# Kernel optimization log

Hardware: AMD Instinct MI355X
Metric: run time of the kernel (lower is better)

Reference implementation:

```python
import jax, jax.numpy as jnp
import numpy as np

NG, ND, NC, H = 100000, 50000, 50000, 128

def _sage(x_src, x_dst, src, dst, n_dst, W_l, b_l, W_r):
    # PyG SAGEConv: lin_l(mean over incoming neighbors of x_src) + lin_r(x_dst)
    msg = x_src[src]                                             # [E, H] gather
    s = jax.ops.segment_sum(msg, dst, num_segments=n_dst)        # [n_dst, H]
    cnt = jax.ops.segment_sum(jnp.ones(src.shape, x_src.dtype), dst, num_segments=n_dst)
    mean = s / jnp.maximum(cnt, 1.0)[:, None]
    return mean @ W_l + b_l + x_dst @ W_r


def setup_inputs() -> dict:
    key = jax.random.key(0)
    ks = jax.random.split(key, 12)
    sc = 1.0 / np.sqrt(H)
    return {
        'emb_gene': jax.random.normal(ks[0], (NG, H), jnp.float32) * 0.02,
        'emb_disease': jax.random.normal(ks[1], (ND, H), jnp.float32) * 0.02,
        'emb_compound': jax.random.normal(ks[2], (NC, H), jnp.float32) * 0.02,
        'Wl': jax.random.normal(ks[3], (2, 4, H, H), jnp.float32) * sc,
        'bl': jnp.zeros((2, 4, H), jnp.float32),
        'Wr': jax.random.normal(ks[4], (2, 4, H, H), jnp.float32) * sc,
        'eg_src': jax.random.randint(ks[5], (600000,), 0, NG),
        'eg_dst': jax.random.randint(ks[6], (600000,), 0, NG),
        'ecd_src': jax.random.randint(ks[7], (300000,), 0, NC),
        'ecd_dst': jax.random.randint(ks[8], (300000,), 0, ND),
        'ecg_src': jax.random.randint(ks[9], (600000,), 0, NC),
        'ecg_dst': jax.random.randint(ks[10], (600000,), 0, NG),
        'egc_src': jax.random.randint(ks[11], (600000,), 0, NG),
        'egc_dst': jax.random.randint(jax.random.fold_in(key, 99), (600000,), 0, NC),
    }


def reference(emb_gene, emb_disease, emb_compound, Wl, bl, Wr,
              eg_src, eg_dst, ecd_src, ecd_dst, ecg_src, ecg_dst, egc_src, egc_dst):
    xg, xd, xc = emb_gene, emb_disease, emb_compound
    for L in range(2):
        # to_hetero with aggr='sum': sum per-relation SAGEConv outputs per dst type
        og = (_sage(xg, xg, eg_src, eg_dst, NG, Wl[L, 0], bl[L, 0], Wr[L, 0]) +
              _sage(xc, xg, ecg_src, ecg_dst, NG, Wl[L, 2], bl[L, 2], Wr[L, 2]))
        od = _sage(xc, xd, ecd_src, ecd_dst, ND, Wl[L, 1], bl[L, 1], Wr[L, 1])
        oc = _sage(xg, xc, egc_src, egc_dst, NC, Wl[L, 3], bl[L, 3], Wr[L, 3])
        if L < 1:  # relu between layers (dropout inactive in eval)
            og, od, oc = jax.nn.relu(og), jax.nn.relu(od), jax.nn.relu(oc)
        xg, xd, xc = og, od, oc
    # concatenate node-type outputs [NG+ND+NC, H] for a single output array
    return jnp.concatenate([xg, xd, xc], axis=0)
```

## Files before the change

kernel.cpp:

```cpp
#include <hip/hip_runtime.h>


constexpr int HD = 128;
constexpr int NBMAX = 512;
constexpr int BSTRIDE = 32768;

typedef __attribute__((ext_vector_type(8))) short bf16x8;
typedef __attribute__((ext_vector_type(16))) float f32x16;
typedef __attribute__((ext_vector_type(2))) float f32x2;

__device__ __forceinline__ unsigned short f2bf(float x) {
  unsigned u = __builtin_bit_cast(unsigned, x);
  u += 0x7FFF + ((u >> 16) & 1);
  return (unsigned short)(u >> 16);
}
__device__ __forceinline__ float bf2f(unsigned short h) {
  return __builtin_bit_cast(float, (unsigned)h << 16);
}

__device__ __forceinline__ uint2 pack_fp8x8(const float* v) {
  uint2 o;
  unsigned t;
  t = (unsigned)__builtin_amdgcn_cvt_pk_fp8_f32(v[0] * 16.f, v[1] * 16.f, 0, false);
  t = (unsigned)__builtin_amdgcn_cvt_pk_fp8_f32(v[2] * 16.f, v[3] * 16.f, (int)t, true);
  o.x = t;
  t = (unsigned)__builtin_amdgcn_cvt_pk_fp8_f32(v[4] * 16.f, v[5] * 16.f, 0, false);
  t = (unsigned)__builtin_amdgcn_cvt_pk_fp8_f32(v[6] * 16.f, v[7] * 16.f, (int)t, true);
  o.y = t;
  return o;
}

__global__ __launch_bounds__(256) void k_convert(const float* __restrict__ s0,
                                                 const float* __restrict__ s1,
                                                 const float* __restrict__ s2,
                                                 unsigned short* __restrict__ d0,
                                                 unsigned short* __restrict__ d1,
                                                 unsigned short* __restrict__ d2,
                                                 unsigned char* __restrict__ e0,
                                                 unsigned char* __restrict__ e2,
                                                 long long n0, long long n1, long long n2) {
  long long i = ((long long)blockIdx.x * 256 + threadIdx.x) * 8;
  const float* s;
  unsigned short* d;
  unsigned char* e;
  if (i < n0) { s = s0 + i; d = d0 + i; e = e0 + i; }
  else if (i < n0 + n1) { s = s1 + (i - n0); d = d1 + (i - n0); e = nullptr; }
  else if (i < n0 + n1 + n2) { s = s2 + (i - n0 - n1); d = d2 + (i - n0 - n1); e = e2 + (i - n0 - n1); }
  else return;
  float4 a = *(const float4*)s;
  float4 b = *(const float4*)(s + 4);
  float v[8] = {a.x, a.y, a.z, a.w, b.x, b.y, b.z, b.w};
  uint4 o;
  o.x = (unsigned)f2bf(v[0]) | ((unsigned)f2bf(v[1]) << 16);
  o.y = (unsigned)f2bf(v[2]) | ((unsigned)f2bf(v[3]) << 16);
  o.z = (unsigned)f2bf(v[4]) | ((unsigned)f2bf(v[5]) << 16);
  o.w = (unsigned)f2bf(v[6]) | ((unsigned)f2bf(v[7]) << 16);
  *(uint4*)d = o;
  if (e) *(uint2*)e = pack_fp8x8(v);
}

struct GArgs {
  const int* esrc[4];
  const int* edst[4];
  int ebase[5];
  int nbase[4];
};

__global__ __launch_bounds__(256) void k_binA(GArgs ga, int Etot, int NB,
                                              int* __restrict__ bucketCur,
                                              unsigned* __restrict__ binned) {
  __shared__ int hist[NBMAX];
  __shared__ int base[NBMAX];
  const int tid = threadIdx.x;
  for (int b = tid; b < NB; b += 256) hist[b] = 0;
  __syncthreads();
  const int e0 = blockIdx.x * 4096;
  for (int i = tid; i < 4096; i += 256) {
    int e = e0 + i;
    if (e < Etot) {
      int r = (e >= ga.ebase[1]) + (e >= ga.ebase[2]) + (e >= ga.ebase[3]);
      int g = ga.nbase[r] + ga.edst[r][e - ga.ebase[r]];
      atomicAdd(&hist[g >> 10], 1);
    }
  }
  __syncthreads();
  for (int b = tid; b < NB; b += 256) {
    int h = hist[b];
    base[b] = h ? atomicAdd(&bucketCur[b], h) : 0;
    hist[b] = 0;
  }
  __syncthreads();
  for (int i = tid; i < 4096; i += 256) {
    int e = e0 + i;
    if (e < Etot) {
      int r = (e >= ga.ebase[1]) + (e >= ga.ebase[2]) + (e >= ga.ebase[3]);
      int el = e - ga.ebase[r];
      int g = ga.nbase[r] + ga.edst[r][el];
      int b = g >> 10;
      int pos = base[b] + atomicAdd(&hist[b], 1);
      binned[(size_t)b * BSTRIDE + pos] =
          ((unsigned)(g & 1023) << 20) | (unsigned)ga.esrc[r][el];
    }
  }
}

__global__ __launch_bounds__(256) void k_binB(const int* __restrict__ bucketCur,
                                              const unsigned* __restrict__ binned,
                                              int* __restrict__ ptr, int* __restrict__ cnt,
                                              int* __restrict__ ss, int Ntot) {
  const int b = blockIdx.x;
  const int tid = threadIdx.x;
  __shared__ int ncnt[1024];
  __shared__ int noff[1024];
  __shared__ int red[256];
  __shared__ int sbase_s;
  __shared__ int wsum[4], wbase[4];

  int part = 0;
  for (int i = tid; i < b; i += 256) part += bucketCur[i];
  red[tid] = part;
  __syncthreads();
  for (int s = 128; s > 0; s >>= 1) {
    if (tid < s) red[tid] += red[tid + s];
    __syncthreads();
  }
  if (tid == 0) sbase_s = red[0];

  for (int j = tid; j < 1024; j += 256) ncnt[j] = 0;
  __syncthreads();

  const int ecount = bucketCur[b];
  const unsigned* bp = binned + (size_t)b * BSTRIDE;
  for (int i = tid; i < ecount; i += 256) atomicAdd(&ncnt[bp[i] >> 20], 1);
  __syncthreads();

  const int j0 = tid * 4;
  int c0 = ncnt[j0], c1 = ncnt[j0 + 1], c2 = ncnt[j0 + 2], c3 = ncnt[j0 + 3];
  int s4 = c0 + c1 + c2 + c3;
  int lane = tid & 63, wid = tid >> 6;
  int incl = s4;
#pragma unroll
  for (int off = 1; off < 64; off <<= 1) {
    int t = __shfl_up(incl, off);
    if (lane >= off) incl += t;
  }
  if (lane == 63) wsum[wid] = incl;
  __syncthreads();
  if (tid == 0) {
    int acc = 0;
#pragma unroll
    for (int w2 = 0; w2 < 4; ++w2) { wbase[w2] = acc; acc += wsum[w2]; }
  }
  __syncthreads();
  int excl = wbase[wid] + incl - s4;
  const int sbase = sbase_s;
  int o0 = excl, o1 = excl + c0, o2 = o1 + c1, o3 = o2 + c2;
  noff[j0] = o0; noff[j0 + 1] = o1; noff[j0 + 2] = o2; noff[j0 + 3] = o3;
  int g0 = b * 1024 + j0;
  if (g0 + 0 < Ntot) { ptr[g0 + 0] = sbase + o0; cnt[g0 + 0] = c0; }
  if (g0 + 1 < Ntot) { ptr[g0 + 1] = sbase + o1; cnt[g0 + 1] = c1; }
  if (g0 + 2 < Ntot) { ptr[g0 + 2] = sbase + o2; cnt[g0 + 2] = c2; }
  if (g0 + 3 < Ntot) { ptr[g0 + 3] = sbase + o3; cnt[g0 + 3] = c3; }
  __syncthreads();

  for (int i = tid; i < ecount; i += 256) {
    unsigned rec = bp[i];
    int j = rec >> 20;
    int p = sbase + atomicAdd(&noff[j], 1);
    ss[p] = (int)(rec & 0xFFFFF);
  }
}

struct AArgs {
  const unsigned char* xs[4];
  unsigned short* mean[4];
  int nbase[4];
  int bbase[5];
  int n[4];
};

__global__ __launch_bounds__(256) void k_aggregate_all(AArgs A, const int* __restrict__ ptr,
                                                       const int* __restrict__ cnt,
                                                       const int* __restrict__ ss) {
  int b = blockIdx.x;
  int r = (b >= A.bbase[1]) + (b >= A.bbase[2]) + (b >= A.bbase[3]);
  int d = (b - A.bbase[r]) * 32 + (threadIdx.x >> 3);
  if (d >= A.n[r]) return;
  const unsigned char* xs = A.xs[r];
  int l = threadIdx.x & 7;
  int g = A.nbase[r] + d;
  int p = ptr[g];
  int deg = cnt[g];
  f32x2 b0 = {0.f, 0.f}, b1 = {0.f, 0.f}, b2 = {0.f, 0.f}, b3 = {0.f, 0.f};
  f32x2 b4 = {0.f, 0.f}, b5 = {0.f, 0.f}, b6 = {0.f, 0.f}, b7 = {0.f, 0.f};
  for (int j0 = 0; j0 < deg; j0 += 8) {
    int m = deg - j0;
    if (m > 8) m = 8;
    int idx = ss[p + j0 + (l < m ? l : m - 1)];
    uint4 uu[8];
#pragma unroll
    for (int k = 0; k < 8; ++k) {
      if (k < m) {
        int s = __shfl(idx, k, 8);
        uu[k] = *(const uint4*)(xs + (size_t)s * HD + l * 16);
      }
    }
#pragma unroll
    for (int k = 0; k < 8; ++k) {
      if (k < m) {
        b0 += __builtin_amdgcn_cvt_pk_f32_fp8(uu[k].x, false);
        b1 += __builtin_amdgcn_cvt_pk_f32_fp8(uu[k].x, true);
        b2 += __builtin_amdgcn_cvt_pk_f32_fp8(uu[k].y, false);
        b3 += __builtin_amdgcn_cvt_pk_f32_fp8(uu[k].y, true);
        b4 += __builtin_amdgcn_cvt_pk_f32_fp8(uu[k].z, false);
        b5 += __builtin_amdgcn_cvt_pk_f32_fp8(uu[k].z, true);
        b6 += __builtin_amdgcn_cvt_pk_f32_fp8(uu[k].w, false);
        b7 += __builtin_amdgcn_cvt_pk_f32_fp8(uu[k].w, true);
      }
    }
  }
  float inv = 1.0f / (16.0f * (float)(deg > 0 ? deg : 1));
  uint4 o;
  unsigned short* mp = A.mean[r] + (size_t)d * HD + l * 16;
  o.x = (unsigned)f2bf(b0.x * inv) | ((unsigned)f2bf(b0.y * inv) << 16);
  o.y = (unsigned)f2bf(b1.x * inv) | ((unsigned)f2bf(b1.y * inv) << 16);
  o.z = (unsigned)f2bf(b2.x * inv) | ((unsigned)f2bf(b2.y * inv) << 16);
  o.w = (unsigned)f2bf(b3.x * inv) | ((unsigned)f2bf(b3.y * inv) << 16);
  *(uint4*)mp = o;
  o.x = (unsigned)f2bf(b4.x * inv) | ((unsigned)f2bf(b4.y * inv) << 16);
  o.y = (unsigned)f2bf(b5.x * inv) | ((unsigned)f2bf(b5.y * inv) << 16);
  o.z = (unsigned)f2bf(b6.x * inv) | ((unsigned)f2bf(b6.y * inv) << 16);
  o.w = (unsigned)f2bf(b7.x * inv) | ((unsigned)f2bf(b7.y * inv) << 16);
  *(uint4*)(mp + 8) = o;
}

struct PrepArgs {
  const float* a[14];
  const float* b[14];
};

__global__ __launch_bounds__(256) void k_prepw(PrepArgs pa, unsigned short* __restrict__ out) {
  int s = blockIdx.x;
  const float* A = pa.a[s];
  const float* B = pa.b[s];
  unsigned short* oh = out + (size_t)s * 16384;
  int e0 = blockIdx.y * 1024 + threadIdx.x * 4;
#pragma unroll
  for (int j = 0; j < 4; ++j) {
    int e = e0 + j;
    int k = e >> 7, n = e & 127;
    float v = A[e] + (B ? B[e] : 0.f);
    oh[n * 128 + (k ^ ((n & 15) << 3))] = f2bf(v);
  }
}

struct GemmArgs {
  const unsigned short* x[3][3];
  const unsigned short* wp[3][3];
  const float* b0[3];
  const float* b1[3];
  float* outf[3];
  unsigned short* outb[3];
  unsigned char* out8[3];
  int M[3];
  int nslab[3];
  int gbase[4];
  int relu;
};

__global__ __launch_bounds__(256, 4) void k_gemm_all(GemmArgs ga) {
  __shared__ unsigned short ldsb[16384];
  const int t = (blockIdx.x >= ga.gbase[1]) + (blockIdx.x >= ga.gbase[2]);
  const int blk = blockIdx.x - ga.gbase[t];
  const int M = ga.M[t];
  const int nslab = ga.nslab[t];
  const int tid = threadIdx.x;
  const int wave = tid >> 6;
  const int lane = tid & 63;
  const int l31 = lane & 31;
  const int lhalf = lane >> 5;

  const int mbase = blk * 128 + wave * 32;
  int r0 = mbase + l31;
  if (r0 > M - 1) r0 = M - 1;

  f32x16 acc[4];
#pragma unroll
  for (int n = 0; n < 4; ++n)
#pragma unroll
    for (int q = 0; q < 16; ++q) acc[n][q] = 0.f;

#pragma unroll
  for (int s = 0; s < 3; ++s) {
    if (s < nslab) {
      const unsigned short* xp = ga.x[t][s] + (size_t)r0 * HD + lhalf * 8;
      bf16x8 areg[8];
#pragma unroll
      for (int ks = 0; ks < 8; ++ks) areg[ks] = *(const bf16x8*)(xp + ks * 16);

      __syncthreads();
      {
        const float4* src = (const float4*)ga.wp[t][s];
        float4* dst = (float4*)ldsb;
#pragma unroll
        for (int j = 0; j < 8; ++j) dst[tid + j * 256] = src[tid + j * 256];
      }
      __syncthreads();

#pragma unroll
      for (int ks = 0; ks < 8; ++ks) {
        const int k0 = ks * 16 + lhalf * 8;
#pragma unroll
        for (int nt = 0; nt < 4; ++nt) {
          const int rown = nt * 32 + l31;
          const int kidx = k0 ^ ((rown & 15) << 3);
          const bf16x8 bb = *(const bf16x8*)&ldsb[rown * HD + kidx];
          acc[nt] = __builtin_amdgcn_mfma_f32_32x32x16_bf16(areg[ks], bb, acc[nt], 0, 0, 0);
        }
      }
    }
  }

  const float* b0 = ga.b0[t];
  const float* b1 = ga.b1[t];
  float* outf = ga.outf[t];
  unsigned short* outb = ga.outb[t];
  unsigned char* out8 = ga.out8[t];
#pragma unroll
  for (int nt = 0; nt < 4; ++nt) {
    const int col = nt * 32 + l31;
    float bias = b0[col] + (b1 ? b1[col] : 0.f);
#pragma unroll
    for (int rg = 0; rg < 16; ++rg) {
      int row = mbase + (rg & 3) + 8 * (rg >> 2) + 4 * lhalf;
      float v = acc[nt][rg] + bias;
      if (ga.relu) v = fmaxf(v, 0.f);
      if (row < M) {
        if (outf) {
          outf[(size_t)row * HD + col] = v;
        } else {
          unsigned short h = f2bf(v);
          outb[(size_t)row * HD + col] = h;
          if (out8) {
            float vb = bf2f(h);
            unsigned pk = (unsigned)__builtin_amdgcn_cvt_pk_fp8_f32(vb * 16.f, vb * 16.f, 0, false);
            out8[(size_t)row * HD + col] = (unsigned char)(pk & 0xFF);
          }
        }
      }
    }
  }
}

extern "C" void kernel_launch(void* const* d_in, const int* in_sizes, int n_in,
                              void* d_out, int out_size, void* d_ws, size_t ws_size,
                              hipStream_t stream) {
  const float* emb_g = (const float*)d_in[0];
  const float* emb_d = (const float*)d_in[1];
  const float* emb_c = (const float*)d_in[2];
  const float* Wl = (const float*)d_in[3];
  const float* bl = (const float*)d_in[4];
  const float* Wr = (const float*)d_in[5];

  const int NG = in_sizes[0] / HD;
  const int ND = in_sizes[1] / HD;
  const int NC = in_sizes[2] / HD;
  const int E0 = in_sizes[6];
  const int E1 = in_sizes[8];
  const int E2 = in_sizes[10];
  const int E3 = in_sizes[12];
  const int HH = HD * HD;
  const int Etot = E0 + E1 + E2 + E3;
  const int Ntot = NG + ND + NG + NC;
  const int NB = (Ntot + 1023) >> 10;

  char* w = (char*)d_ws;
  unsigned short* wprep = (unsigned short*)w; w += (size_t)14 * 32768;
  unsigned short* xbf_g0 = (unsigned short*)w; w += (size_t)NG * HD * 2;
  unsigned short* xbf_d0 = (unsigned short*)w; w += (size_t)ND * HD * 2;
  unsigned short* xbf_c0 = (unsigned short*)w; w += (size_t)NC * HD * 2;
  unsigned short* xbf_g1 = (unsigned short*)w; w += (size_t)NG * HD * 2;
  unsigned short* xbf_d1 = (unsigned short*)w; w += (size_t)ND * HD * 2;
  unsigned short* xbf_c1 = (unsigned short*)w; w += (size_t)NC * HD * 2;
  unsigned short* mean_gg = (unsigned short*)w; w += (size_t)NG * HD * 2;
  unsigned short* mean_cd = (unsigned short*)w; w += (size_t)ND * HD * 2;
  unsigned short* mean_cg = (unsigned short*)w; w += (size_t)NG * HD * 2;
  unsigned short* mean_gc = (unsigned short*)w; w += (size_t)NC * HD * 2;
  unsigned char* x8_g0 = (unsigned char*)w; w += (size_t)NG * HD;
  unsigned char* x8_c0 = (unsigned char*)w; w += (size_t)NC * HD;
  unsigned char* x8_g1 = (unsigned char*)w; w += (size_t)NG * HD;
  unsigned char* x8_c1 = (unsigned char*)w; w += (size_t)NC * HD;
  int* ss = (int*)w;        w += (size_t)Etot * 4;
  int* ptr = (int*)w;       w += (size_t)Ntot * 4;
  int* cnt = (int*)w;       w += (size_t)Ntot * 4;
  unsigned* binned = (unsigned*)w; w += (size_t)NB * BSTRIDE * 4;
  int* bucketCur = (int*)w; w += (size_t)NBMAX * 4;

  hipMemsetAsync(bucketCur, 0, (size_t)NBMAX * 4, stream);

  {
    long long n0 = (long long)NG * HD, n1 = (long long)ND * HD, n2 = (long long)NC * HD;
    long long tot8 = (n0 + n1 + n2) / 8;
    k_convert<<<(int)((tot8 + 255) / 256), 256, 0, stream>>>(
        emb_g, emb_d, emb_c, xbf_g0, xbf_d0, xbf_c0, x8_g0, x8_c0, n0, n1, n2);
  }

  GArgs ga;
  ga.esrc[0] = (const int*)d_in[6];  ga.edst[0] = (const int*)d_in[7];
  ga.esrc[1] = (const int*)d_in[8];  ga.edst[1] = (const int*)d_in[9];
  ga.esrc[2] = (const int*)d_in[10]; ga.edst[2] = (const int*)d_in[11];
  ga.esrc[3] = (const int*)d_in[12]; ga.edst[3] = (const int*)d_in[13];
  ga.ebase[0] = 0; ga.ebase[1] = E0; ga.ebase[2] = E0 + E1;
  ga.ebase[3] = E0 + E1 + E2; ga.ebase[4] = Etot;
  ga.nbase[0] = 0; ga.nbase[1] = NG; ga.nbase[2] = NG + ND; ga.nbase[3] = NG + ND + NG;

  k_binA<<<(Etot + 4095) / 4096, 256, 0, stream>>>(ga, Etot, NB, bucketCur, binned);
  k_binB<<<NB, 256, 0, stream>>>(bucketCur, binned, ptr, cnt, ss, Ntot);

  PrepArgs pa;
  for (int L = 0; L < 2; ++L) {
    int b = L * 7;
    pa.a[b + 0] = Wl + (size_t)(L * 4 + 0) * HH; pa.b[b + 0] = nullptr;
    pa.a[b + 1] = Wl + (size_t)(L * 4 + 2) * HH; pa.b[b + 1] = nullptr;
    pa.a[b + 2] = Wr + (size_t)(L * 4 + 0) * HH; pa.b[b + 2] = Wr + (size_t)(L * 4 + 2) * HH;
    pa.a[b + 3] = Wl + (size_t)(L * 4 + 1) * HH; pa.b[b + 3] = nullptr;
    pa.a[b + 4] = Wr + (size_t)(L * 4 + 1) * HH; pa.b[b + 4] = nullptr;
    pa.a[b + 5] = Wl + (size_t)(L * 4 + 3) * HH; pa.b[b + 5] = nullptr;
    pa.a[b + 6] = Wr + (size_t)(L * 4 + 3) * HH; pa.b[b + 6] = nullptr;
  }
  k_prepw<<<dim3(14, 16), 256, 0, stream>>>(pa, wprep);

  float* out = (float*)d_out;
  float* xg_out = out;
  float* xd_out = out + (size_t)NG * HD;
  float* xc_out = out + (size_t)(NG + ND) * HD;

  for (int L = 0; L < 2; ++L) {
    const unsigned short* xg = L ? xbf_g1 : xbf_g0;
    const unsigned short* xd = L ? xbf_d1 : xbf_d0;
    const unsigned short* xc = L ? xbf_c1 : xbf_c0;
    const unsigned char* x8g = L ? x8_g1 : x8_g0;
    const unsigned char* x8c = L ? x8_c1 : x8_c0;

    AArgs aa;
    aa.xs[0] = x8g; aa.xs[1] = x8c; aa.xs[2] = x8c; aa.xs[3] = x8g;
    aa.mean[0] = mean_gg; aa.mean[1] = mean_cd; aa.mean[2] = mean_cg; aa.mean[3] = mean_gc;
    aa.nbase[0] = 0; aa.nbase[1] = NG; aa.nbase[2] = NG + ND; aa.nbase[3] = NG + ND + NG;
    aa.n[0] = NG; aa.n[1] = ND; aa.n[2] = NG; aa.n[3] = NC;
    int bb = 0;
    for (int r = 0; r < 4; ++r) { aa.bbase[r] = bb; bb += (aa.n[r] + 31) / 32; }
    aa.bbase[4] = bb;
    k_aggregate_all<<<bb, 256, 0, stream>>>(aa, ptr, cnt, ss);

    const float* bl_L = bl + (size_t)L * 4 * HD;
    const unsigned short* wp = wprep + (size_t)L * 7 * 16384;

    GemmArgs gm;
    gm.x[0][0] = mean_gg; gm.x[0][1] = mean_cg; gm.x[0][2] = xg;
    gm.wp[0][0] = wp + 0 * 16384; gm.wp[0][1] = wp + 1 * 16384; gm.wp[0][2] = wp + 2 * 16384;
    gm.b0[0] = bl_L + 0 * HD; gm.b1[0] = bl_L + 2 * HD;
    gm.M[0] = NG; gm.nslab[0] = 3;
    gm.x[1][0] = mean_cd; gm.x[1][1] = xd; gm.x[1][2] = nullptr;
    gm.wp[1][0] = wp + 3 * 16384; gm.wp[1][1] = wp + 4 * 16384; gm.wp[1][2] = nullptr;
    gm.b0[1] = bl_L + 1 * HD; gm.b1[1] = nullptr;
    gm.M[1] = ND; gm.nslab[1] = 2;
    gm.x[2][0] = mean_gc; gm.x[2][1] = xc; gm.x[2][2] = nullptr;
    gm.wp[2][0] = wp + 5 * 16384; gm.wp[2][1] = wp + 6 * 16384; gm.wp[2][2] = nullptr;
    gm.b0[2] = bl_L + 3 * HD; gm.b1[2] = nullptr;
    gm.M[2] = NC; gm.nslab[2] = 2;
    if (L) {
      gm.outf[0] = xg_out; gm.outf[1] = xd_out; gm.outf[2] = xc_out;
      gm.outb[0] = gm.outb[1] = gm.outb[2] = nullptr;
      gm.out8[0] = gm.out8[1] = gm.out8[2] = nullptr;
    } else {
      gm.outf[0] = gm.outf[1] = gm.outf[2] = nullptr;
      gm.outb[0] = xbf_g1; gm.outb[1] = xbf_d1; gm.outb[2] = xbf_c1;
      gm.out8[0] = x8_g1; gm.out8[1] = nullptr; gm.out8[2] = x8_c1;
    }
    gm.relu = (L == 0) ? 1 : 0;
    int gb = 0;
    for (int t = 0; t < 3; ++t) { gm.gbase[t] = gb; gb += (gm.M[t] + 127) / 128; }
    gm.gbase[3] = gb;
    k_gemm_all<<<gb, 256, 0, stream>>>(gm);
  }
}
```

Measured before the change: 334.1 us.

## Fuse front-end kernels, pad CSR segments for vectorized index loads

Merges the embedding conversion, edge binning pass A, and weight prep into a single k_front launch distinguished by block ranges, removing two launches and letting them overlap. The CSR built in k_binB now pads each node's neighbor segment to a multiple of 8 and aligns each bucket base, so the aggregation kernel can read 8 source indices with two uint4 loads instead of a strided load plus shuffles. Aggregated mean rows are written with nontemporal stores. The padding enlarges the index buffer and reads slightly past valid entries for partial groups, which are masked by m.

After: 331.8 us. No clear change (-0.7%).

```diff
diff --git a/kernel.cpp b/kernel.cpp
--- a/kernel.cpp
+++ b/kernel.cpp
@@ -4,10 +4,12 @@
 constexpr int HD = 128;
 constexpr int NBMAX = 512;
 constexpr int BSTRIDE = 32768;
+constexpr int PADRES = 7176;
 
 typedef __attribute__((ext_vector_type(8))) short bf16x8;
 typedef __attribute__((ext_vector_type(16))) float f32x16;
 typedef __attribute__((ext_vector_type(2))) float f32x2;
+typedef __attribute__((ext_vector_type(4))) unsigned int u32x4;
 
 __device__ __forceinline__ unsigned short f2bf(float x) {
   unsigned u = __builtin_bit_cast(unsigned, x);
@@ -30,35 +32,6 @@
   return o;
 }
 
-__global__ __launch_bounds__(256) void k_convert(const float* __restrict__ s0,
-                                                 const float* __restrict__ s1,
-                                                 const float* __restrict__ s2,
-                                                 unsigned short* __restrict__ d0,
-                                                 unsigned short* __restrict__ d1,
-                                                 unsigned short* __restrict__ d2,
-                                                 unsigned char* __restrict__ e0,
-                                                 unsigned char* __restrict__ e2,
-                                                 long long n0, long long n1, long long n2) {
-  long long i = ((long long)blockIdx.x * 256 + threadIdx.x) * 8;
-  const float* s;
-  unsigned short* d;
-  unsigned char* e;
-  if (i < n0) { s = s0 + i; d = d0 + i; e = e0 + i; }
-  else if (i < n0 + n1) { s = s1 + (i - n0); d = d1 + (i - n0); e = nullptr; }
-  else if (i < n0 + n1 + n2) { s = s2 + (i - n0 - n1); d = d2 + (i - n0 - n1); e = e2 + (i - n0 - n1); }
-  else return;
-  float4 a = *(const float4*)s;
-  float4 b = *(const float4*)(s + 4);
-  float v[8] = {a.x, a.y, a.z, a.w, b.x, b.y, b.z, b.w};
-  uint4 o;
-  o.x = (unsigned)f2bf(v[0]) | ((unsigned)f2bf(v[1]) << 16);
-  o.y = (unsigned)f2bf(v[2]) | ((unsigned)f2bf(v[3]) << 16);
-  o.z = (unsigned)f2bf(v[4]) | ((unsigned)f2bf(v[5]) << 16);
-  o.w = (unsigned)f2bf(v[6]) | ((unsigned)f2bf(v[7]) << 16);
-  *(uint4*)d = o;
-  if (e) *(uint2*)e = pack_fp8x8(v);
-}
-
 struct GArgs {
   const int* esrc[4];
   const int* edst[4];
@@ -66,41 +39,102 @@
   int nbase[4];
 };
 
-__global__ __launch_bounds__(256) void k_binA(GArgs ga, int Etot, int NB,
-                                              int* __restrict__ bucketCur,
-                                              unsigned* __restrict__ binned) {
+struct PrepArgs {
+  const float* a[14];
+  const float* b[14];
+};
+
+struct FrontArgs {
+  const float *cs0, *cs1, *cs2;
+  unsigned short *cd0, *cd1, *cd2;
+  unsigned char *ce0, *ce2;
+  long long n0, n1, n2;
+  GArgs ga;
+  int Etot, NB;
+  int* bucketCur;
+  unsigned* binned;
+  PrepArgs pa;
+  unsigned short* wprep;
+  int cb, ab;
+};
+
+__global__ __launch_bounds__(256) void k_front(FrontArgs f) {
   __shared__ int hist[NBMAX];
   __shared__ int base[NBMAX];
   const int tid = threadIdx.x;
-  for (int b = tid; b < NB; b += 256) hist[b] = 0;
-  __syncthreads();
-  const int e0 = blockIdx.x * 4096;
-  for (int i = tid; i < 4096; i += 256) {
-    int e = e0 + i;
-    if (e < Etot) {
-      int r = (e >= ga.ebase[1]) + (e >= ga.ebase[2]) + (e >= ga.ebase[3]);
-      int g = ga.nbase[r] + ga.edst[r][e - ga.ebase[r]];
-      atomicAdd(&hist[g >> 10], 1);
-    }
-  }
-  __syncthreads();
-  for (int b = tid; b < NB; b += 256) {
-    int h = hist[b];
-    base[b] = h ? atomicAdd(&bucketCur[b], h) : 0;
-    hist[b] = 0;
-  }
-  __syncthreads();
-  for (int i = tid; i < 4096; i += 256) {
-    int e = e0 + i;
-    if (e < Etot) {
-      int r = (e >= ga.ebase[1]) + (e >= ga.ebase[2]) + (e >= ga.ebase[3]);
-      int el = e - ga.ebase[r];
-      int g = ga.nbase[r] + ga.edst[r][el];
-      int b = g >> 10;
-      int pos = base[b] + atomicAdd(&hist[b], 1);
-      binned[(size_t)b * BSTRIDE + pos] =
-          ((unsigned)(g & 1023) << 20) | (unsigned)ga.esrc[r][el];
-    }
+  int b = blockIdx.x;
+
+  if (b < f.cb) {
+    long long i = ((long long)b * 256 + tid) * 8;
+    const float* s;
+    unsigned short* d;
+    unsigned char* e;
+    if (i < f.n0) { s = f.cs0 + i; d = f.cd0 + i; e = f.ce0 + i; }
+    else if (i < f.n0 + f.n1) { s = f.cs1 + (i - f.n0); d = f.cd1 + (i - f.n0); e = nullptr; }
+    else if (i < f.n0 + f.n1 + f.n2) {
+      long long o2 = i - f.n0 - f.n1;
+      s = f.cs2 + o2; d = f.cd2 + o2; e = f.ce2 + o2;
+    } else return;
+    float4 a = *(const float4*)s;
+    float4 bb = *(const float4*)(s + 4);
+    float v[8] = {a.x, a.y, a.z, a.w, bb.x, bb.y, bb.z, bb.w};
+    uint4 o;
+    o.x = (unsigned)f2bf(v[0]) | ((unsigned)f2bf(v[1]) << 16);
+    o.y = (unsigned)f2bf(v[2]) | ((unsigned)f2bf(v[3]) << 16);
+    o.z = (unsigned)f2bf(v[4]) | ((unsigned)f2bf(v[5]) << 16);
+    o.w = (unsigned)f2bf(v[6]) | ((unsigned)f2bf(v[7]) << 16);
+    *(uint4*)d = o;
+    if (e) *(uint2*)e = pack_fp8x8(v);
+    return;
+  }
+  b -= f.cb;
+
+  if (b < f.ab) {
+    for (int j = tid; j < f.NB; j += 256) hist[j] = 0;
+    __syncthreads();
+    const int e0 = b * 4096;
+    for (int i = tid; i < 4096; i += 256) {
+      int e = e0 + i;
+      if (e < f.Etot) {
+        int r = (e >= f.ga.ebase[1]) + (e >= f.ga.ebase[2]) + (e >= f.ga.ebase[3]);
+        int g = f.ga.nbase[r] + f.ga.edst[r][e - f.ga.ebase[r]];
+        atomicAdd(&hist[g >> 10], 1);
+      }
+    }
+    __syncthreads();
+    for (int j = tid; j < f.NB; j += 256) {
+      int h = hist[j];
+      base[j] = h ? atomicAdd(&f.bucketCur[j], h) : 0;
+      hist[j] = 0;
+    }
+    __syncthreads();
+    for (int i = tid; i < 4096; i += 256) {
+      int e = e0 + i;
+      if (e < f.Etot) {
+        int r = (e >= f.ga.ebase[1]) + (e >= f.ga.ebase[2]) + (e >= f.ga.ebase[3]);
+        int el = e - f.ga.ebase[r];
+        int g = f.ga.nbase[r] + f.ga.edst[r][el];
+        int bk = g >> 10;
+        int pos = base[bk] + atomicAdd(&hist[bk], 1);
+        f.binned[(size_t)bk * BSTRIDE + pos] =
+            ((unsigned)(g & 1023) << 20) | (unsigned)f.ga.esrc[r][el];
+      }
+    }
+    return;
+  }
+  b -= f.ab;
+
+  int s = b >> 4, y = b & 15;
+  const float* A = f.pa.a[s];
+  const float* B = f.pa.b[s];
+  unsigned short* oh = f.wprep + (size_t)s * 16384;
+  int e0 = y * 1024 + tid * 4;
+#pragma unroll
+  for (int j = 0; j < 4; ++j) {
+    int e = e0 + j;
+    int k = e >> 7, n = e & 127;
+    float v = A[e] + (B ? B[e] : 0.f);
+    oh[n * 128 + (k ^ ((n & 15) << 3))] = f2bf(v);
   }
 }
 
@@ -124,7 +158,7 @@
     if (tid < s) red[tid] += red[tid + s];
     __syncthreads();
   }
-  if (tid == 0) sbase_s = red[0];
+  if (tid == 0) sbase_s = ((red[0] + 7) & ~7) + b * PADRES;
 
   for (int j = tid; j < 1024; j += 256) ncnt[j] = 0;
   __syncthreads();
@@ -136,7 +170,8 @@
 
   const int j0 = tid * 4;
   int c0 = ncnt[j0], c1 = ncnt[j0 + 1], c2 = ncnt[j0 + 2], c3 = ncnt[j0 + 3];
-  int s4 = c0 + c1 + c2 + c3;
+  int p0 = (c0 + 7) & ~7, p1 = (c1 + 7) & ~7, p2 = (c2 + 7) & ~7, p3 = (c3 + 7) & ~7;
+  int s4 = p0 + p1 + p2 + p3;
   int lane = tid & 63, wid = tid >> 6;
   int incl = s4;
 #pragma unroll
@@ -154,7 +189,7 @@
   __syncthreads();
   int excl = wbase[wid] + incl - s4;
   const int sbase = sbase_s;
-  int o0 = excl, o1 = excl + c0, o2 = o1 + c1, o3 = o2 + c2;
+  int o0 = excl, o1 = o0 + p0, o2 = o1 + p1, o3 = o2 + p2;
   noff[j0] = o0; noff[j0 + 1] = o1; noff[j0 + 2] = o2; noff[j0 + 3] = o3;
   int g0 = b * 1024 + j0;
   if (g0 + 0 < Ntot) { ptr[g0 + 0] = sbase + o0; cnt[g0 + 0] = c0; }
@@ -196,15 +231,18 @@
   for (int j0 = 0; j0 < deg; j0 += 8) {
     int m = deg - j0;
     if (m > 8) m = 8;
-    int idx = ss[p + j0 + (l < m ? l : m - 1)];
+    const uint4* ip = (const uint4*)(ss + p + j0);
+    uint4 ia = ip[0];
+    uint4 ib = ip[1];
     uint4 uu[8];
-#pragma unroll
-    for (int k = 0; k < 8; ++k) {
-      if (k < m) {
-        int s = __shfl(idx, k, 8);
-        uu[k] = *(const uint4*)(xs + (size_t)s * HD + l * 16);
-      }
-    }
+    if (m > 0) uu[0] = *(const uint4*)(xs + (size_t)ia.x * HD + l * 16);
+    if (m > 1) uu[1] = *(const uint4*)(xs + (size_t)ia.y * HD + l * 16);
+    if (m > 2) uu[2] = *(const uint4*)(xs + (size_t)ia.z * HD + l * 16);
+    if (m > 3) uu[3] = *(const uint4*)(xs + (size_t)ia.w * HD + l * 16);
+    if (m > 4) uu[4] = *(const uint4*)(xs + (size_t)ib.x * HD + l * 16);
+    if (m > 5) uu[5] = *(const uint4*)(xs + (size_t)ib.y * HD + l * 16);
+    if (m > 6) uu[6] = *(const uint4*)(xs + (size_t)ib.z * HD + l * 16);
+    if (m > 7) uu[7] = *(const uint4*)(xs + (size_t)ib.w * HD + l * 16);
 #pragma unroll
     for (int k = 0; k < 8; ++k) {
       if (k < m) {
@@ -220,38 +258,18 @@
     }
   }
   float inv = 1.0f / (16.0f * (float)(deg > 0 ? deg : 1));
-  uint4 o;
+  u32x4 o;
   unsigned short* mp = A.mean[r] + (size_t)d * HD + l * 16;
   o.x = (unsigned)f2bf(b0.x * inv) | ((unsigned)f2bf(b0.y * inv) << 16);
   o.y = (unsigned)f2bf(b1.x * inv) | ((unsigned)f2bf(b1.y * inv) << 16);
   o.z = (unsigned)f2bf(b2.x * inv) | ((unsigned)f2bf(b2.y * inv) << 16);
   o.w = (unsigned)f2bf(b3.x * inv) | ((unsigned)f2bf(b3.y * inv) << 16);
-  *(uint4*)mp = o;
+  __builtin_nontemporal_store(o, (u32x4*)mp);
   o.x = (unsigned)f2bf(b4.x * inv) | ((unsigned)f2bf(b4.y * inv) << 16);
   o.y = (unsigned)f2bf(b5.x * inv) | ((unsigned)f2bf(b5.y * inv) << 16);
   o.z = (unsigned)f2bf(b6.x * inv) | ((unsigned)f2bf(b6.y * inv) << 16);
   o.w = (unsigned)f2bf(b7.x * inv) | ((unsigned)f2bf(b7.y * inv) << 16);
-  *(uint4*)(mp + 8) = o;
-}
-
-struct PrepArgs {
-  const float* a[14];
-  const float* b[14];
-};
-
-__global__ __launch_bounds__(256) void k_prepw(PrepArgs pa, unsigned short* __restrict__ out) {
-  int s = blockIdx.x;
-  const float* A = pa.a[s];
-  const float* B = pa.b[s];
-  unsigned short* oh = out + (size_t)s * 16384;
-  int e0 = blockIdx.y * 1024 + threadIdx.x * 4;
-#pragma unroll
-  for (int j = 0; j < 4; ++j) {
-    int e = e0 + j;
-    int k = e >> 7, n = e & 127;
-    float v = A[e] + (B ? B[e] : 0.f);
-    oh[n * 128 + (k ^ ((n & 15) << 3))] = f2bf(v);
-  }
+  __builtin_nontemporal_store(o, (u32x4*)(mp + 8));
 }
 
 struct GemmArgs {
@@ -390,7 +408,7 @@
   unsigned char* x8_c0 = (unsigned char*)w; w += (size_t)NC * HD;
   unsigned char* x8_g1 = (unsigned char*)w; w += (size_t)NG * HD;
   unsigned char* x8_c1 = (unsigned char*)w; w += (size_t)NC * HD;
-  int* ss = (int*)w;        w += (size_t)Etot * 4;
+  int* ss = (int*)w;        w += ((size_t)Etot + (size_t)NB * PADRES + 64) * 4;
   int* ptr = (int*)w;       w += (size_t)Ntot * 4;
   int* cnt = (int*)w;       w += (size_t)Ntot * 4;
   unsigned* binned = (unsigned*)w; w += (size_t)NB * BSTRIDE * 4;
@@ -398,37 +416,37 @@
 
   hipMemsetAsync(bucketCur, 0, (size_t)NBMAX * 4, stream);
 
-  {
-    long long n0 = (long long)NG * HD, n1 = (long long)ND * HD, n2 = (long long)NC * HD;
-    long long tot8 = (n0 + n1 + n2) / 8;
-    k_convert<<<(int)((tot8 + 255) / 256), 256, 0, stream>>>(
-        emb_g, emb_d, emb_c, xbf_g0, xbf_d0, xbf_c0, x8_g0, x8_c0, n0, n1, n2);
-  }
-
-  GArgs ga;
-  ga.esrc[0] = (const int*)d_in[6];  ga.edst[0] = (const int*)d_in[7];
-  ga.esrc[1] = (const int*)d_in[8];  ga.edst[1] = (const int*)d_in[9];
-  ga.esrc[2] = (const int*)d_in[10]; ga.edst[2] = (const int*)d_in[11];
-  ga.esrc[3] = (const int*)d_in[12]; ga.edst[3] = (const int*)d_in[13];
-  ga.ebase[0] = 0; ga.ebase[1] = E0; ga.ebase[2] = E0 + E1;
-  ga.ebase[3] = E0 + E1 + E2; ga.ebase[4] = Etot;
-  ga.nbase[0] = 0; ga.nbase[1] = NG; ga.nbase[2] = NG + ND; ga.nbase[3] = NG + ND + NG;
-
-  k_binA<<<(Etot + 4095) / 4096, 256, 0, stream>>>(ga, Etot, NB, bucketCur, binned);
-  k_binB<<<NB, 256, 0, stream>>>(bucketCur, binned, ptr, cnt, ss, Ntot);
-
-  PrepArgs pa;
+  FrontArgs fa;
+  fa.cs0 = emb_g; fa.cs1 = emb_d; fa.cs2 = emb_c;
+  fa.cd0 = xbf_g0; fa.cd1 = xbf_d0; fa.cd2 = xbf_c0;
+  fa.ce0 = x8_g0; fa.ce2 = x8_c0;
+  fa.n0 = (long long)NG * HD; fa.n1 = (long long)ND * HD; fa.n2 = (long long)NC * HD;
+  fa.ga.esrc[0] = (const int*)d_in[6];  fa.ga.edst[0] = (const int*)d_in[7];
+  fa.ga.esrc[1] = (const int*)d_in[8];  fa.ga.edst[1] = (const int*)d_in[9];
+  fa.ga.esrc[2] = (const int*)d_in[10]; fa.ga.edst[2] = (const int*)d_in[11];
+  fa.ga.esrc[3] = (const int*)d_in[12]; fa.ga.edst[3] = (const int*)d_in[13];
+  fa.ga.ebase[0] = 0; fa.ga.ebase[1] = E0; fa.ga.ebase[2] = E0 + E1;
+  fa.ga.ebase[3] = E0 + E1 + E2; fa.ga.ebase[4] = Etot;
+  fa.ga.nbase[0] = 0; fa.ga.nbase[1] = NG; fa.ga.nbase[2] = NG + ND; fa.ga.nbase[3] = NG + ND + NG;
+  fa.Etot = Etot; fa.NB = NB;
+  fa.bucketCur = bucketCur; fa.binned = binned;
   for (int L = 0; L < 2; ++L) {
     int b = L * 7;
-    pa.a[b + 0] = Wl + (size_t)(L * 4 + 0) * HH; pa.b[b + 0] = nullptr;
-    pa.a[b + 1] = Wl + (size_t)(L * 4 + 2) * HH; pa.b[b + 1] = nullptr;
-    pa.a[b + 2] = Wr + (size_t)(L * 4 + 0) * HH; pa.b[b + 2] = Wr + (size_t)(L * 4 + 2) * HH;
-    pa.a[b + 3] = Wl + (size_t)(L * 4 + 1) * HH; pa.b[b + 3] = nullptr;
-    pa.a[b + 4] = Wr + (size_t)(L * 4 + 1) * HH; pa.b[b + 4] = nullptr;
-    pa.a[b + 5] = Wl + (size_t)(L * 4 + 3) * HH; pa.b[b + 5] = nullptr;
-    pa.a[b + 6] = Wr + (size_t)(L * 4 + 3) * HH; pa.b[b + 6] = nullptr;
-  }
-  k_prepw<<<dim3(14, 16), 256, 0, stream>>>(pa, wprep);
+    fa.pa.a[b + 0] = Wl + (size_t)(L * 4 + 0) * HH; fa.pa.b[b + 0] = nullptr;
+    fa.pa.a[b + 1] = Wl + (size_t)(L * 4 + 2) * HH; fa.pa.b[b + 1] = nullptr;
+    fa.pa.a[b + 2] = Wr + (size_t)(L * 4 + 0) * HH; fa.pa.b[b + 2] = Wr + (size_t)(L * 4 + 2) * HH;
+    fa.pa.a[b + 3] = Wl + (size_t)(L * 4 + 1) * HH; fa.pa.b[b + 3] = nullptr;
+    fa.pa.a[b + 4] = Wr + (size_t)(L * 4 + 1) * HH; fa.pa.b[b + 4] = nullptr;
+    fa.pa.a[b + 5] = Wl + (size_t)(L * 4 + 3) * HH; fa.pa.b[b + 5] = nullptr;
+    fa.pa.a[b + 6] = Wr + (size_t)(L * 4 + 3) * HH; fa.pa.b[b + 6] = nullptr;
+  }
+  fa.wprep = wprep;
+  long long tot8 = (fa.n0 + fa.n1 + fa.n2) / 8;
+  fa.cb = (int)((tot8 + 255) / 256);
+  fa.ab = (Etot + 4095) / 4096;
+  k_front<<<fa.cb + fa.ab + 14 * 16, 256, 0, stream>>>(fa);
+
+  k_binB<<<NB, 256, 0, stream>>>(bucketCur, binned, ptr, cnt, ss, Ntot);
 
   float* out = (float*)d_out;
   float* xg_out = out;
```

## Shard bucket counters, pad per-node edge lists, vector-load neighbor indices

Applied to the files above, without the earlier changes.

The binning pass now spreads each bucket's global atomic counter over 8 slots with separate sub-regions, rotates the bucket visiting order per block, and processes 8192 edges per block, all to cut atomic contention on the bucket counters. The CSR layout pads each node's neighbor list to a multiple of 8 and aligns each bucket base, so the aggregate kernel can fetch 8 source indices with two uint4 loads instead of a load plus shuffles. The mean outputs are written with nontemporal stores. In exchange the index array grows with padding, and each sub-slot is capped at 4096 edges per bucket, which could overflow on skewed inputs.

After: 364.6 us. +9.1%, slower.

```diff
diff --git a/kernel.cpp b/kernel.cpp
--- a/kernel.cpp
+++ b/kernel.cpp
@@ -4,10 +4,14 @@
 constexpr int HD = 128;
 constexpr int NBMAX = 512;
 constexpr int BSTRIDE = 32768;
+constexpr int SUBSTRIDE = 4096;
+constexpr int EPB = 8192;
+constexpr int PADRES = 7176;
 
 typedef __attribute__((ext_vector_type(8))) short bf16x8;
 typedef __attribute__((ext_vector_type(16))) float f32x16;
 typedef __attribute__((ext_vector_type(2))) float f32x2;
+typedef __attribute__((ext_vector_type(4))) unsigned int u32x4;
 
 __device__ __forceinline__ unsigned short f2bf(float x) {
   unsigned u = __builtin_bit_cast(unsigned, x);
@@ -72,10 +76,11 @@
   __shared__ int hist[NBMAX];
   __shared__ int base[NBMAX];
   const int tid = threadIdx.x;
-  for (int b = tid; b < NB; b += 256) hist[b] = 0;
-  __syncthreads();
-  const int e0 = blockIdx.x * 4096;
-  for (int i = tid; i < 4096; i += 256) {
+  const int slot = blockIdx.x & 7;
+  for (int j = tid; j < NB; j += 256) hist[j] = 0;
+  __syncthreads();
+  const int e0 = blockIdx.x * EPB;
+  for (int i = tid; i < EPB; i += 256) {
     int e = e0 + i;
     if (e < Etot) {
       int r = (e >= ga.ebase[1]) + (e >= ga.ebase[2]) + (e >= ga.ebase[3]);
@@ -84,21 +89,23 @@
     }
   }
   __syncthreads();
-  for (int b = tid; b < NB; b += 256) {
-    int h = hist[b];
-    base[b] = h ? atomicAdd(&bucketCur[b], h) : 0;
-    hist[b] = 0;
-  }
-  __syncthreads();
-  for (int i = tid; i < 4096; i += 256) {
+  const int roff = (int)((blockIdx.x * 67u) % (unsigned)NB);
+  for (int j = tid; j < NB; j += 256) {
+    int jj = j + roff; if (jj >= NB) jj -= NB;
+    int h = hist[jj];
+    base[jj] = h ? atomicAdd(&bucketCur[slot * NBMAX + jj], h) : 0;
+    hist[jj] = 0;
+  }
+  __syncthreads();
+  for (int i = tid; i < EPB; i += 256) {
     int e = e0 + i;
     if (e < Etot) {
       int r = (e >= ga.ebase[1]) + (e >= ga.ebase[2]) + (e >= ga.ebase[3]);
       int el = e - ga.ebase[r];
       int g = ga.nbase[r] + ga.edst[r][el];
-      int b = g >> 10;
-      int pos = base[b] + atomicAdd(&hist[b], 1);
-      binned[(size_t)b * BSTRIDE + pos] =
+      int bk = g >> 10;
+      int pos = base[bk] + atomicAdd(&hist[bk], 1);
+      binned[(size_t)bk * BSTRIDE + slot * SUBSTRIDE + pos] =
           ((unsigned)(g & 1023) << 20) | (unsigned)ga.esrc[r][el];
     }
   }
@@ -117,26 +124,32 @@
   __shared__ int wsum[4], wbase[4];
 
   int part = 0;
-  for (int i = tid; i < b; i += 256) part += bucketCur[i];
+#pragma unroll
+  for (int s = 0; s < 8; ++s)
+    for (int i = tid; i < b; i += 256) part += bucketCur[s * NBMAX + i];
   red[tid] = part;
   __syncthreads();
   for (int s = 128; s > 0; s >>= 1) {
     if (tid < s) red[tid] += red[tid + s];
     __syncthreads();
   }
-  if (tid == 0) sbase_s = red[0];
+  if (tid == 0) sbase_s = ((red[0] + 7) & ~7) + b * PADRES;
 
   for (int j = tid; j < 1024; j += 256) ncnt[j] = 0;
   __syncthreads();
 
-  const int ecount = bucketCur[b];
-  const unsigned* bp = binned + (size_t)b * BSTRIDE;
-  for (int i = tid; i < ecount; i += 256) atomicAdd(&ncnt[bp[i] >> 20], 1);
+#pragma unroll
+  for (int s = 0; s < 8; ++s) {
+    int c = bucketCur[s * NBMAX + b];
+    const unsigned* bps = binned + (size_t)b * BSTRIDE + s * SUBSTRIDE;
+    for (int i = tid; i < c; i += 256) atomicAdd(&ncnt[bps[i] >> 20], 1);
+  }
   __syncthreads();
 
   const int j0 = tid * 4;
   int c0 = ncnt[j0], c1 = ncnt[j0 + 1], c2 = ncnt[j0 + 2], c3 = ncnt[j0 + 3];
-  int s4 = c0 + c1 + c2 + c3;
+  int p0 = (c0 + 7) & ~7, p1 = (c1 + 7) & ~7, p2 = (c2 + 7) & ~7, p3 = (c3 + 7) & ~7;
+  int s4 = p0 + p1 + p2 + p3;
   int lane = tid & 63, wid = tid >> 6;
   int incl = s4;
 #pragma unroll
@@ -154,7 +167,7 @@
   __syncthreads();
   int excl = wbase[wid] + incl - s4;
   const int sbase = sbase_s;
-  int o0 = excl, o1 = excl + c0, o2 = o1 + c1, o3 = o2 + c2;
+  int o0 = excl, o1 = o0 + p0, o2 = o1 + p1, o3 = o2 + p2;
   noff[j0] = o0; noff[j0 + 1] = o1; noff[j0 + 2] = o2; noff[j0 + 3] = o3;
   int g0 = b * 1024 + j0;
   if (g0 + 0 < Ntot) { ptr[g0 + 0] = sbase + o0; cnt[g0 + 0] = c0; }
@@ -163,11 +176,36 @@
   if (g0 + 3 < Ntot) { ptr[g0 + 3] = sbase + o3; cnt[g0 + 3] = c3; }
   __syncthreads();
 
-  for (int i = tid; i < ecount; i += 256) {
-    unsigned rec = bp[i];
-    int j = rec >> 20;
-    int p = sbase + atomicAdd(&noff[j], 1);
-    ss[p] = (int)(rec & 0xFFFFF);
+#pragma unroll
+  for (int s = 0; s < 8; ++s) {
+    int c = bucketCur[s * NBMAX + b];
+    const unsigned* bps = binned + (size_t)b * BSTRIDE + s * SUBSTRIDE;
+    for (int i = tid; i < c; i += 256) {
+      unsigned rec = bps[i];
+      int j = rec >> 20;
+      int p = sbase + atomicAdd(&noff[j], 1);
+      ss[p] = (int)(rec & 0xFFFFF);
+    }
+  }
+}
+
+struct PrepArgs {
+  const float* a[14];
+  const float* b[14];
+};
+
+__global__ __launch_bounds__(256) void k_prepw(PrepArgs pa, unsigned short* __restrict__ out) {
+  int s = blockIdx.x;
+  const float* A = pa.a[s];
+  const float* B = pa.b[s];
+  unsigned short* oh = out + (size_t)s * 16384;
+  int e0 = blockIdx.y * 1024 + threadIdx.x * 4;
+#pragma unroll
+  for (int j = 0; j < 4; ++j) {
+    int e = e0 + j;
+    int k = e >> 7, n = e & 127;
+    float v = A[e] + (B ? B[e] : 0.f);
+    oh[n * 128 + (k ^ ((n & 15) << 3))] = f2bf(v);
   }
 }
 
@@ -196,15 +234,18 @@
   for (int j0 = 0; j0 < deg; j0 += 8) {
     int m = deg - j0;
     if (m > 8) m = 8;
-    int idx = ss[p + j0 + (l < m ? l : m - 1)];
+    const uint4* ip = (const uint4*)(ss + p + j0);
+    uint4 ia = ip[0];
+    uint4 ib = ip[1];
     uint4 uu[8];
-#pragma unroll
-    for (int k = 0; k < 8; ++k) {
-      if (k < m) {
-        int s = __shfl(idx, k, 8);
-        uu[k] = *(const uint4*)(xs + (size_t)s * HD + l * 16);
-      }
-    }
+    if (m > 0) uu[0] = *(const uint4*)(xs + (size_t)ia.x * HD + l * 16);
+    if (m > 1) uu[1] = *(const uint4*)(xs + (size_t)ia.y * HD + l * 16);
+    if (m > 2) uu[2] = *(const uint4*)(xs + (size_t)ia.z * HD + l * 16);
+    if (m > 3) uu[3] = *(const uint4*)(xs + (size_t)ia.w * HD + l * 16);
+    if (m > 4) uu[4] = *(const uint4*)(xs + (size_t)ib.x * HD + l * 16);
+    if (m > 5) uu[5] = *(const uint4*)(xs + (size_t)ib.y * HD + l * 16);
+    if (m > 6) uu[6] = *(const uint4*)(xs + (size_t)ib.z * HD + l * 16);
+    if (m > 7) uu[7] = *(const uint4*)(xs + (size_t)ib.w * HD + l * 16);
 #pragma unroll
     for (int k = 0; k < 8; ++k) {
       if (k < m) {
@@ -220,38 +261,18 @@
     }
   }
   float inv = 1.0f / (16.0f * (float)(deg > 0 ? deg : 1));
-  uint4 o;
+  u32x4 o;
   unsigned short* mp = A.mean[r] + (size_t)d * HD + l * 16;
   o.x = (unsigned)f2bf(b0.x * inv) | ((unsigned)f2bf(b0.y * inv) << 16);
   o.y = (unsigned)f2bf(b1.x * inv) | ((unsigned)f2bf(b1.y * inv) << 16);
   o.z = (unsigned)f2bf(b2.x * inv) | ((unsigned)f2bf(b2.y * inv) << 16);
   o.w = (unsigned)f2bf(b3.x * inv) | ((unsigned)f2bf(b3.y * inv) << 16);
-  *(uint4*)mp = o;
+  __builtin_nontemporal_store(o, (u32x4*)mp);
   o.x = (unsigned)f2bf(b4.x * inv) | ((unsigned)f2bf(b4.y * inv) << 16);
   o.y = (unsigned)f2bf(b5.x * inv) | ((unsigned)f2bf(b5.y * inv) << 16);
   o.z = (unsigned)f2bf(b6.x * inv) | ((unsigned)f2bf(b6.y * inv) << 16);
   o.w = (unsigned)f2bf(b7.x * inv) | ((unsigned)f2bf(b7.y * inv) << 16);
-  *(uint4*)(mp + 8) = o;
-}
-
-struct PrepArgs {
-  const float* a[14];
-  const float* b[14];
-};
-
-__global__ __launch_bounds__(256) void k_prepw(PrepArgs pa, unsigned short* __restrict__ out) {
-  int s = blockIdx.x;
-  const float* A = pa.a[s];
-  const float* B = pa.b[s];
-  unsigned short* oh = out + (size_t)s * 16384;
-  int e0 = blockIdx.y * 1024 + threadIdx.x * 4;
-#pragma unroll
-  for (int j = 0; j < 4; ++j) {
-    int e = e0 + j;
-    int k = e >> 7, n = e & 127;
-    float v = A[e] + (B ? B[e] : 0.f);
-    oh[n * 128 + (k ^ ((n & 15) << 3))] = f2bf(v);
-  }
+  __builtin_nontemporal_store(o, (u32x4*)(mp + 8));
 }
 
 struct GemmArgs {
@@ -390,13 +411,13 @@
   unsigned char* x8_c0 = (unsigned char*)w; w += (size_t)NC * HD;
   unsigned char* x8_g1 = (unsigned char*)w; w += (size_t)NG * HD;
   unsigned char* x8_c1 = (unsigned char*)w; w += (size_t)NC * HD;
-  int* ss = (int*)w;        w += (size_t)Etot * 4;
+  int* ss = (int*)w;        w += ((size_t)Etot + (size_t)NB * PADRES + 64) * 4;
   int* ptr = (int*)w;       w += (size_t)Ntot * 4;
   int* cnt = (int*)w;       w += (size_t)Ntot * 4;
   unsigned* binned = (unsigned*)w; w += (size_t)NB * BSTRIDE * 4;
-  int* bucketCur = (int*)w; w += (size_t)NBMAX * 4;
-
-  hipMemsetAsync(bucketCur, 0, (size_t)NBMAX * 4, stream);
+  int* bucketCur = (int*)w; w += (size_t)8 * NBMAX * 4;
+
+  hipMemsetAsync(bucketCur, 0, (size_t)8 * NBMAX * 4, stream);
 
   {
     long long n0 = (long long)NG * HD, n1 = (long long)ND * HD, n2 = (long long)NC * HD;
@@ -414,7 +435,7 @@
   ga.ebase[3] = E0 + E1 + E2; ga.ebase[4] = Etot;
   ga.nbase[0] = 0; ga.nbase[1] = NG; ga.nbase[2] = NG + ND; ga.nbase[3] = NG + ND + NG;
 
-  k_binA<<<(Etot + 4095) / 4096, 256, 0, stream>>>(ga, Etot, NB, bucketCur, binned);
+  k_binA<<<(Etot + EPB - 1) / EPB, 256, 0, stream>>>(ga, Etot, NB, bucketCur, binned);
   k_binB<<<NB, 256, 0, stream>>>(bucketCur, binned, ptr, cnt, ss, Ntot);
 
   PrepArgs pa;
```
